# Kernel tuning notes

Hardware: AMD Instinct MI355X
Metric: run time of the kernel (lower is better)

Reference implementation:

```python
import jax, jax.numpy as jnp
import numpy as np


def setup_inputs() -> dict:
    key = jax.random.key(0)
    k0, k1, k2, k3 = jax.random.split(key, 4)
    B, C_IN, H, W = 8, 256, 64, 64
    O, NUM = 256, 8  # output channels, number of regions
    mat0 = jax.random.normal(k0, (B, C_IN, H, W), dtype=jnp.float32)
    mat1 = jax.random.normal(k1, (O, C_IN, NUM), dtype=jnp.float32)  # per-region 1x1 filters (shared across batch, batch_W=1)
    mask = jax.random.uniform(k2, (NUM, H, W), dtype=jnp.float32)    # soft region weights per pixel
    Alpha = jax.random.uniform(k3, (NUM,), dtype=jnp.float32)        # per-region modulation scale
    return {"mat0": mat0, "mat1": mat1, "mask": mask, "Alpha": Alpha, "use_alpha": 1, "beta": 1}


def reference(mat0, mat1, mask, Alpha, use_alpha, beta):
    # Deformable (region-aware) matmul: for each pixel (h,w), apply the
    # region-r filter mat1[:, :, r] to mat0[:, :, h, w], weighted by the
    # per-pixel soft region mask (optionally alpha-modulated per region).
    # out[b,o,h,w] = sum_r sum_c mat0[b,c,h,w] * mat1[o,c,r] * Alpha[r] * mask[r,h,w]
    m1 = mat1 * Alpha if use_alpha else mat1  # [O, C, R] scaled per region
    return jnp.einsum('bchw,ocr,rhw->bohw', mat0, m1, mask)
```

## Files before the change

### kernel.cpp

```cpp
#include <hip/hip_runtime.h>
#include <hip/hip_bf16.h>
#include <stdint.h>


typedef __attribute__((ext_vector_type(8)))  _Float16 half8;
typedef __attribute__((ext_vector_type(16))) float    f32x16;

#define C_IN  256
#define HW_   4096
#define NRND  32

__global__ __launch_bounds__(256) void prep_w_kernel(
    const float* __restrict__ mat1, const float* __restrict__ Alpha,
    const int* __restrict__ use_alpha, _Float16* __restrict__ Aprep) {
  int t = blockIdx.x * 256 + threadIdx.x;
  int o = t & 255;
  int c = t >> 8;
  int ua = use_alpha[0];
  const float* src = mat1 + ((size_t)o * C_IN + c) * 8;
  half8 v;
#pragma unroll
  for (int r = 0; r < 8; ++r) {
    float s = ua ? Alpha[r] : 1.0f;
    v[r] = (_Float16)(src[r] * s);
  }
  *(half8*)(Aprep + ((size_t)c * 256 + o) * 8) = v;
}

__global__ __launch_bounds__(256, 2) void gemm_deform_kernel(
    const float* __restrict__ mat0, const _Float16* __restrict__ Aprep,
    const float* __restrict__ mask, float* __restrict__ out) {
  __shared__ half8 A_lds[4][1024];

  int bid = blockIdx.x;
  int wg = (bid & 7) * 64 + (bid >> 3);
  int tile_m = wg & 1;
  int tile_n = wg >> 1;
  int o0 = tile_m * 128;
  int n0 = tile_n * 128;
  int b  = n0 >> 12;
  int p0 = n0 & 4095;

  int t    = threadIdx.x;
  int lane = t & 63;
  int w    = t >> 6;
  int wc   = w & 1;
  int wr   = w >> 1;
  int l31  = lane & 31;
  int cr   = lane >> 5;

  int colb = p0 + wc * 64 + l31;
  half8 mkh0, mkh1;
#pragma unroll
  for (int r = 0; r < 8; ++r) {
    mkh0[r] = (_Float16)mask[r * HW_ + colb];
    mkh1[r] = (_Float16)mask[r * HW_ + colb + 32];
  }

  const float* __restrict__ m0b =
      mat0 + ((size_t)b * C_IN + cr) * HW_ + colb;

  const __attribute__((address_space(1))) uint32_t* gA =
      (const __attribute__((address_space(1))) uint32_t*)Aprep;
  __attribute__((address_space(3))) uint32_t* lA =
      (__attribute__((address_space(3))) uint32_t*)&A_lds[0][0];
  int soo  = (w & 1) * 64 + lane;
  int scqb = w >> 1;
  const __attribute__((address_space(1))) uint32_t* gS0 =
      gA + (size_t)((0 * 2 + scqb) * 256 + o0 + soo) * 4;
  const __attribute__((address_space(1))) uint32_t* gS1 =
      gA + (size_t)((1 * 2 + scqb) * 256 + o0 + soo) * 4;
  const __attribute__((address_space(1))) uint32_t* gS2 =
      gA + (size_t)((2 * 2 + scqb) * 256 + o0 + soo) * 4;
  const __attribute__((address_space(1))) uint32_t* gS3 =
      gA + (size_t)((3 * 2 + scqb) * 256 + o0 + soo) * 4;
  const float* pP0 = m0b + (size_t)0 * HW_;
  const float* pP1 = m0b + (size_t)2 * HW_;
  const float* pP2 = m0b + (size_t)4 * HW_;
  const float* pP3 = m0b + (size_t)6 * HW_;

#define STAGE(SLAB, SB) do {                                                  \
    __builtin_amdgcn_global_load_lds(gS0, lA + ((SLAB)*1024 + 0*256 + w*64)*4, 16, 0, 0); \
    __builtin_amdgcn_global_load_lds(gS1, lA + ((SLAB)*1024 + 1*256 + w*64)*4, 16, 0, 0); \
    __builtin_amdgcn_global_load_lds(gS2, lA + ((SLAB)*1024 + 2*256 + w*64)*4, 16, 0, 0); \
    __builtin_amdgcn_global_load_lds(gS3, lA + ((SLAB)*1024 + 3*256 + w*64)*4, 16, 0, 0); \
    gS0 += (SB); gS1 += (SB); gS2 += (SB); gS3 += (SB);                       \
  } while (0)

  f32x16 acc00, acc01, acc10, acc11;
#pragma unroll
  for (int j = 0; j < 16; ++j) { acc00[j] = 0.f; acc01[j] = 0.f; acc10[j] = 0.f; acc11[j] = 0.f; }

  float Pev[4][2], Pod[4][2];

  auto SM = [&](float s0, float s1, half8 A0, half8 A1) {
    _Float16 h0 = (_Float16)s0, h1 = (_Float16)s1;
    half8 pb0 = {h0, h0, h0, h0, h0, h0, h0, h0};
    half8 pb1 = {h1, h1, h1, h1, h1, h1, h1, h1};
    half8 bv0 = pb0 * mkh0;
    half8 bv1 = pb1 * mkh1;
    acc00 = __builtin_amdgcn_mfma_f32_32x32x16_f16(A0, bv0, acc00, 0, 0, 0);
    acc01 = __builtin_amdgcn_mfma_f32_32x32x16_f16(A0, bv1, acc01, 0, 0, 0);
    acc10 = __builtin_amdgcn_mfma_f32_32x32x16_f16(A1, bv0, acc10, 0, 0, 0);
    acc11 = __builtin_amdgcn_mfma_f32_32x32x16_f16(A1, bv1, acc11, 0, 0, 0);
  };

  int abase = wr * 64 + l31;

  auto COMP = [&](const half8* __restrict__ Ab, float (&P)[4][2], int PB) {
    half8 a0 = Ab[(0 + cr) * 128 + abase];
    half8 a1 = Ab[(0 + cr) * 128 + abase + 32];
    half8 b0 = Ab[(2 + cr) * 128 + abase];
    half8 b1 = Ab[(2 + cr) * 128 + abase + 32];
    SM(P[0][0], P[0][1], a0, a1);
    P[0][0] = pP0[0]; P[0][1] = pP0[32]; pP0 += PB;
    a0 = Ab[(4 + cr) * 128 + abase];
    a1 = Ab[(4 + cr) * 128 + abase + 32];
    SM(P[1][0], P[1][1], b0, b1);
    P[1][0] = pP1[0]; P[1][1] = pP1[32]; pP1 += PB;
    b0 = Ab[(6 + cr) * 128 + abase];
    b1 = Ab[(6 + cr) * 128 + abase + 32];
    SM(P[2][0], P[2][1], a0, a1);
    P[2][0] = pP2[0]; P[2][1] = pP2[32]; pP2 += PB;
    SM(P[3][0], P[3][1], b0, b1);
    P[3][0] = pP3[0]; P[3][1] = pP3[32]; pP3 += PB;
  };

  STAGE(0, 8192);
  STAGE(1, 8192);
  Pev[0][0] = pP0[0]; Pev[0][1] = pP0[32]; pP0 += 8 * HW_;
  Pev[1][0] = pP1[0]; Pev[1][1] = pP1[32]; pP1 += 8 * HW_;
  Pev[2][0] = pP2[0]; Pev[2][1] = pP2[32]; pP2 += 8 * HW_;
  Pev[3][0] = pP3[0]; Pev[3][1] = pP3[32]; pP3 += 8 * HW_;
  Pod[0][0] = pP0[0]; Pod[0][1] = pP0[32]; pP0 += 8 * HW_;
  Pod[1][0] = pP1[0]; Pod[1][1] = pP1[32]; pP1 += 8 * HW_;
  Pod[2][0] = pP2[0]; Pod[2][1] = pP2[32]; pP2 += 8 * HW_;
  Pod[3][0] = pP3[0]; Pod[3][1] = pP3[32]; pP3 += 8 * HW_;

#pragma unroll 1
  for (int g = 0; g < 8; ++g) {
    int rd = g * 4;
    asm volatile("s_waitcnt vmcnt(0)" ::: "memory");
    __builtin_amdgcn_s_barrier();
    {
      int sb2 = (rd + 2 < 31) ? 8192 : 0;
      int sb3 = (rd + 3 < 31) ? 8192 : 0;
      int pb2 = (rd + 2 < 31) ? 8 * HW_ : 0;
      int pb3 = (rd + 3 < 31) ? 8 * HW_ : 0;
      STAGE(2, sb2);
      STAGE(3, sb3);
      COMP(&A_lds[0][0], Pev, pb2);
      COMP(&A_lds[1][0], Pod, pb3);
    }
    asm volatile("s_waitcnt vmcnt(0)" ::: "memory");
    __builtin_amdgcn_s_barrier();
    {
      int sb4 = (rd + 4 < 31) ? 8192 : 0;
      int sb5 = (rd + 5 < 31) ? 8192 : 0;
      int pb4 = (rd + 4 < 31) ? 8 * HW_ : 0;
      int pb5 = (rd + 5 < 31) ? 8 * HW_ : 0;
      STAGE(0, sb4);
      STAGE(1, sb5);
      COMP(&A_lds[2][0], Pev, pb4);
      COMP(&A_lds[3][0], Pod, pb5);
    }
  }

  size_t obase = (size_t)b * 256 * HW_ + colb;
#pragma unroll
  for (int reg = 0; reg < 16; ++reg) {
    int row = o0 + wr * 64 + (reg & 3) + 8 * (reg >> 2) + 4 * cr;
    out[obase + (size_t)row * HW_]                    = acc00[reg];
    out[obase + (size_t)row * HW_ + 32]               = acc01[reg];
    out[obase + (size_t)(row + 32) * HW_]             = acc10[reg];
    out[obase + (size_t)(row + 32) * HW_ + 32]        = acc11[reg];
  }
}

extern "C" void kernel_launch(void* const* d_in, const int* in_sizes, int n_in,
                              void* d_out, int out_size, void* d_ws, size_t ws_size,
                              hipStream_t stream) {
  const float* mat0      = (const float*)d_in[0];
  const float* mat1      = (const float*)d_in[1];
  const float* mask      = (const float*)d_in[2];
  const float* Alpha     = (const float*)d_in[3];
  const int*   use_alpha = (const int*)d_in[4];
  (void)in_sizes; (void)n_in; (void)out_size; (void)ws_size;

  _Float16* Aprep = (_Float16*)d_ws;
  float* outp  = (float*)d_out;

  prep_w_kernel<<<256, 256, 0, stream>>>(mat1, Alpha, use_alpha, Aprep);
  gemm_deform_kernel<<<512, 256, 0, stream>>>(mat0, Aprep, mask, outp);
}
```

Measured before the change: 47.98 us.

## Use 8 waves per block with 64x32 warp tiles and relaxed vmcnt waits

Doubles the workgroup to 512 threads (8 waves), so each wave computes a 64x32 output tile with two MFMA accumulators instead of four. A-slab staging is split across more threads, with two global_load_lds per thread instead of four. The waitcnt before each barrier is relaxed from vmcnt(0) to vmcnt(8) so mat0 prefetch loads can stay in flight. This raises the wave count to hide memory latency but halves per-wave reuse of the LDS A fragments. The vmcnt(8) wait relies on the order of outstanding loads to guarantee the LDS slabs have landed, which risks a correctness hazard.

Result: no change. 48.81 us (+1.7%).

```diff
diff --git a/kernel.cpp b/kernel.cpp
--- a/kernel.cpp
+++ b/kernel.cpp
@@ -8,7 +8,6 @@
 
 #define C_IN  256
 #define HW_   4096
-#define NRND  32
 
 __global__ __launch_bounds__(256) void prep_w_kernel(
     const float* __restrict__ mat1, const float* __restrict__ Alpha,
@@ -27,7 +26,7 @@
   *(half8*)(Aprep + ((size_t)c * 256 + o) * 8) = v;
 }
 
-__global__ __launch_bounds__(256, 2) void gemm_deform_kernel(
+__global__ __launch_bounds__(512, 4) void gemm_deform_kernel(
     const float* __restrict__ mat0, const _Float16* __restrict__ Aprep,
     const float* __restrict__ mask, float* __restrict__ out) {
   __shared__ half8 A_lds[4][1024];
@@ -44,103 +43,89 @@
   int t    = threadIdx.x;
   int lane = t & 63;
   int w    = t >> 6;
-  int wc   = w & 1;
-  int wr   = w >> 1;
+  int wc   = w & 3;
+  int wr   = w >> 2;
   int l31  = lane & 31;
   int cr   = lane >> 5;
 
-  int colb = p0 + wc * 64 + l31;
-  half8 mkh0, mkh1;
+  int colb = p0 + wc * 32 + l31;
+  half8 mkh;
 #pragma unroll
-  for (int r = 0; r < 8; ++r) {
-    mkh0[r] = (_Float16)mask[r * HW_ + colb];
-    mkh1[r] = (_Float16)mask[r * HW_ + colb + 32];
-  }
-
-  const float* __restrict__ m0b =
-      mat0 + ((size_t)b * C_IN + cr) * HW_ + colb;
+  for (int r = 0; r < 8; ++r) mkh[r] = (_Float16)mask[r * HW_ + colb];
 
   const __attribute__((address_space(1))) uint32_t* gA =
       (const __attribute__((address_space(1))) uint32_t*)Aprep;
   __attribute__((address_space(3))) uint32_t* lA =
       (__attribute__((address_space(3))) uint32_t*)&A_lds[0][0];
-  int soo  = (w & 1) * 64 + lane;
-  int scqb = w >> 1;
+  int srow = t & 127;
+  int scq  = t >> 7;
   const __attribute__((address_space(1))) uint32_t* gS0 =
-      gA + (size_t)((0 * 2 + scqb) * 256 + o0 + soo) * 4;
+      gA + (size_t)(scq * 256 + o0 + srow) * 4;
   const __attribute__((address_space(1))) uint32_t* gS1 =
-      gA + (size_t)((1 * 2 + scqb) * 256 + o0 + soo) * 4;
-  const __attribute__((address_space(1))) uint32_t* gS2 =
-      gA + (size_t)((2 * 2 + scqb) * 256 + o0 + soo) * 4;
-  const __attribute__((address_space(1))) uint32_t* gS3 =
-      gA + (size_t)((3 * 2 + scqb) * 256 + o0 + soo) * 4;
+      gA + (size_t)((4 + scq) * 256 + o0 + srow) * 4;
+  const float* __restrict__ m0b =
+      mat0 + ((size_t)b * C_IN + cr) * HW_ + colb;
   const float* pP0 = m0b + (size_t)0 * HW_;
   const float* pP1 = m0b + (size_t)2 * HW_;
   const float* pP2 = m0b + (size_t)4 * HW_;
   const float* pP3 = m0b + (size_t)6 * HW_;
 
 #define STAGE(SLAB, SB) do {                                                  \
-    __builtin_amdgcn_global_load_lds(gS0, lA + ((SLAB)*1024 + 0*256 + w*64)*4, 16, 0, 0); \
-    __builtin_amdgcn_global_load_lds(gS1, lA + ((SLAB)*1024 + 1*256 + w*64)*4, 16, 0, 0); \
-    __builtin_amdgcn_global_load_lds(gS2, lA + ((SLAB)*1024 + 2*256 + w*64)*4, 16, 0, 0); \
-    __builtin_amdgcn_global_load_lds(gS3, lA + ((SLAB)*1024 + 3*256 + w*64)*4, 16, 0, 0); \
-    gS0 += (SB); gS1 += (SB); gS2 += (SB); gS3 += (SB);                       \
+    __builtin_amdgcn_global_load_lds(gS0, lA + (size_t)((SLAB)*1024 + t) * 4,       16, 0, 0); \
+    __builtin_amdgcn_global_load_lds(gS1, lA + (size_t)((SLAB)*1024 + 512 + t) * 4, 16, 0, 0); \
+    gS0 += (SB); gS1 += (SB);                                                 \
   } while (0)
 
-  f32x16 acc00, acc01, acc10, acc11;
+  f32x16 acc0, acc1;
 #pragma unroll
-  for (int j = 0; j < 16; ++j) { acc00[j] = 0.f; acc01[j] = 0.f; acc10[j] = 0.f; acc11[j] = 0.f; }
+  for (int j = 0; j < 16; ++j) { acc0[j] = 0.f; acc1[j] = 0.f; }
 
-  float Pev[4][2], Pod[4][2];
+  float Pev[4], Pod[4];
 
-  auto SM = [&](float s0, float s1, half8 A0, half8 A1) {
-    _Float16 h0 = (_Float16)s0, h1 = (_Float16)s1;
-    half8 pb0 = {h0, h0, h0, h0, h0, h0, h0, h0};
-    half8 pb1 = {h1, h1, h1, h1, h1, h1, h1, h1};
-    half8 bv0 = pb0 * mkh0;
-    half8 bv1 = pb1 * mkh1;
-    acc00 = __builtin_amdgcn_mfma_f32_32x32x16_f16(A0, bv0, acc00, 0, 0, 0);
-    acc01 = __builtin_amdgcn_mfma_f32_32x32x16_f16(A0, bv1, acc01, 0, 0, 0);
-    acc10 = __builtin_amdgcn_mfma_f32_32x32x16_f16(A1, bv0, acc10, 0, 0, 0);
-    acc11 = __builtin_amdgcn_mfma_f32_32x32x16_f16(A1, bv1, acc11, 0, 0, 0);
+  auto SM = [&](float s, half8 A0, half8 A1) {
+    _Float16 h = (_Float16)s;
+    half8 pb = {h, h, h, h, h, h, h, h};
+    half8 bv = pb * mkh;
+    acc0 = __builtin_amdgcn_mfma_f32_32x32x16_f16(A0, bv, acc0, 0, 0, 0);
+    acc1 = __builtin_amdgcn_mfma_f32_32x32x16_f16(A1, bv, acc1, 0, 0, 0);
   };
 
   int abase = wr * 64 + l31;
 
-  auto COMP = [&](const half8* __restrict__ Ab, float (&P)[4][2], int PB) {
+  auto COMP = [&](const half8* __restrict__ Ab, float (&P)[4], int PB) {
     half8 a0 = Ab[(0 + cr) * 128 + abase];
     half8 a1 = Ab[(0 + cr) * 128 + abase + 32];
     half8 b0 = Ab[(2 + cr) * 128 + abase];
     half8 b1 = Ab[(2 + cr) * 128 + abase + 32];
-    SM(P[0][0], P[0][1], a0, a1);
-    P[0][0] = pP0[0]; P[0][1] = pP0[32]; pP0 += PB;
+    SM(P[0], a0, a1);
+    P[0] = pP0[0]; pP0 += PB;
     a0 = Ab[(4 + cr) * 128 + abase];
     a1 = Ab[(4 + cr) * 128 + abase + 32];
-    SM(P[1][0], P[1][1], b0, b1);
-    P[1][0] = pP1[0]; P[1][1] = pP1[32]; pP1 += PB;
+    SM(P[1], b0, b1);
+    P[1] = pP1[0]; pP1 += PB;
     b0 = Ab[(6 + cr) * 128 + abase];
     b1 = Ab[(6 + cr) * 128 + abase + 32];
-    SM(P[2][0], P[2][1], a0, a1);
-    P[2][0] = pP2[0]; P[2][1] = pP2[32]; pP2 += PB;
-    SM(P[3][0], P[3][1], b0, b1);
-    P[3][0] = pP3[0]; P[3][1] = pP3[32]; pP3 += PB;
+    SM(P[2], a0, a1);
+    P[2] = pP2[0]; pP2 += PB;
+    SM(P[3], b0, b1);
+    P[3] = pP3[0]; pP3 += PB;
   };
 
   STAGE(0, 8192);
   STAGE(1, 8192);
-  Pev[0][0] = pP0[0]; Pev[0][1] = pP0[32]; pP0 += 8 * HW_;
-  Pev[1][0] = pP1[0]; Pev[1][1] = pP1[32]; pP1 += 8 * HW_;
-  Pev[2][0] = pP2[0]; Pev[2][1] = pP2[32]; pP2 += 8 * HW_;
-  Pev[3][0] = pP3[0]; Pev[3][1] = pP3[32]; pP3 += 8 * HW_;
-  Pod[0][0] = pP0[0]; Pod[0][1] = pP0[32]; pP0 += 8 * HW_;
-  Pod[1][0] = pP1[0]; Pod[1][1] = pP1[32]; pP1 += 8 * HW_;
-  Pod[2][0] = pP2[0]; Pod[2][1] = pP2[32]; pP2 += 8 * HW_;
-  Pod[3][0] = pP3[0]; Pod[3][1] = pP3[32]; pP3 += 8 * HW_;
+  Pev[0] = pP0[0]; pP0 += 8 * HW_;
+  Pev[1] = pP1[0]; pP1 += 8 * HW_;
+  Pev[2] = pP2[0]; pP2 += 8 * HW_;
+  Pev[3] = pP3[0]; pP3 += 8 * HW_;
+  Pod[0] = pP0[0]; pP0 += 8 * HW_;
+  Pod[1] = pP1[0]; pP1 += 8 * HW_;
+  Pod[2] = pP2[0]; pP2 += 8 * HW_;
+  Pod[3] = pP3[0]; pP3 += 8 * HW_;
 
 #pragma unroll 1
   for (int g = 0; g < 8; ++g) {
     int rd = g * 4;
-    asm volatile("s_waitcnt vmcnt(0)" ::: "memory");
+    asm volatile("s_waitcnt vmcnt(8)" ::: "memory");
     __builtin_amdgcn_s_barrier();
     {
       int sb2 = (rd + 2 < 31) ? 8192 : 0;
@@ -152,7 +137,7 @@
       COMP(&A_lds[0][0], Pev, pb2);
       COMP(&A_lds[1][0], Pod, pb3);
     }
-    asm volatile("s_waitcnt vmcnt(0)" ::: "memory");
+    asm volatile("s_waitcnt vmcnt(8)" ::: "memory");
     __builtin_amdgcn_s_barrier();
     {
       int sb4 = (rd + 4 < 31) ? 8192 : 0;
@@ -170,10 +155,8 @@
 #pragma unroll
   for (int reg = 0; reg < 16; ++reg) {
     int row = o0 + wr * 64 + (reg & 3) + 8 * (reg >> 2) + 4 * cr;
-    out[obase + (size_t)row * HW_]                    = acc00[reg];
-    out[obase + (size_t)row * HW_ + 32]               = acc01[reg];
-    out[obase + (size_t)(row + 32) * HW_]             = acc10[reg];
-    out[obase + (size_t)(row + 32) * HW_ + 32]        = acc11[reg];
+    out[obase + (size_t)row * HW_]        = acc0[reg];
+    out[obase + (size_t)(row + 32) * HW_] = acc1[reg];
   }
 }
 
@@ -191,5 +174,5 @@
   float* outp  = (float*)d_out;
 
   prep_w_kernel<<<256, 256, 0, stream>>>(mat1, Alpha, use_alpha, Aprep);
-  gemm_deform_kernel<<<512, 256, 0, stream>>>(mat0, Aprep, mask, outp);
+  gemm_deform_kernel<<<512, 512, 0, stream>>>(mat0, Aprep, mask, outp);
 }
```
